# Performance work log

Hardware: AMD Instinct MI355X
Metric: run time of the kernel (lower is better)

Reference implementation:

```python
import jax, jax.numpy as jnp
import numpy as np

B, LK, H = 32, 4096, 512

def setup_inputs() -> dict:
    key = jax.random.key(0)
    ks = jax.random.split(key, 9)
    s = 1.0 / np.sqrt(H)
    return {
        "query": jax.random.normal(ks[0], (B, 1, H), jnp.float32),
        "keys": jax.random.normal(ks[1], (B, LK, H), jnp.float32),
        "Wa_w": jax.random.uniform(ks[2], (H, H), jnp.float32, -s, s),
        "Wa_b": jax.random.uniform(ks[3], (H,), jnp.float32, -s, s),
        "Ua_w": jax.random.uniform(ks[4], (H, H), jnp.float32, -s, s),
        "Ua_b": jax.random.uniform(ks[5], (H,), jnp.float32, -s, s),
        "Va_w": jax.random.uniform(ks[6], (1, H), jnp.float32, -s, s),
        "Va_b": jax.random.uniform(ks[7], (1,), jnp.float32, -s, s),
        "temperature": jnp.ones((1,), jnp.float32),
        "valid_src_len": jax.random.randint(ks[8], (B,), 1, LK + 1, jnp.int32),
    }

def reference(query, keys, Wa_w, Wa_b, Ua_w, Ua_b, Va_w, Va_b, temperature, valid_src_len):
    Lk = keys.shape[1]
    q = query @ Wa_w.T + Wa_b                      # [B,1,H]
    k = keys @ Ua_w.T + Ua_b                       # [B,Lk,H]
    # additive score: Va(tanh(Wa q + Ua k)) / T -> [B,Lk,1]
    scores = (jnp.tanh(q + k) @ Va_w.T + Va_b) / temperature
    scores = scores[..., 0][:, None, :]            # [B,1,Lk]
    mask = jnp.arange(Lk)[None, None, :] < valid_src_len[:, None, None]
    scores = jnp.where(mask, scores, jnp.asarray(-1e9, scores.dtype))
    weights = jax.nn.softmax(scores, axis=-1)      # [B,1,Lk]
    context = jnp.einsum('bql,blh->bqh', weights, keys)  # [B,1,H]
    return context, weights
```

## Files before the change

### kernel.cpp

```cpp
#include <hip/hip_runtime.h>

#define B_SZ 32
#define LK   4096
#define H    512
#define MT   64
#define AST  1040

typedef __bf16 bf16x8 __attribute__((ext_vector_type(8)));
typedef float  f32x4  __attribute__((ext_vector_type(4)));

__device__ inline unsigned short f2bf_rne(float f) {
    unsigned int u = __float_as_uint(f);
    u += 0x7FFFu + ((u >> 16) & 1u);
    return (unsigned short)(u >> 16);
}
__device__ inline unsigned pack_trunc(float lo, float hi) {
    return __builtin_amdgcn_perm(__float_as_uint(hi), __float_as_uint(lo), 0x07060302u);
}
__device__ inline float tanh_fast(float x) {
    float e = __expf(2.0f * x);
    return 1.0f - 2.0f * __builtin_amdgcn_rcpf(e + 1.0f);
}

__global__ void cvt_ua_kernel(const float* __restrict__ Ua_w, unsigned short* __restrict__ ua_t) {
    int n = blockIdx.x;
    int t = threadIdx.x;
    float2 f = *(const float2*)(Ua_w + n * H + t * 2);
    unsigned w = (unsigned)f2bf_rne(f.x) | ((unsigned)f2bf_rne(f.y) << 16);
    int k8 = t >> 2, off = t & 3;
    *(unsigned*)(ua_t + (size_t)k8 * (H * 8) + n * 8 + off * 2) = w;
}

__global__ void qproj_kernel(const float* __restrict__ query, const float* __restrict__ Wa_w,
                             const float* __restrict__ Wa_b, const float* __restrict__ Ua_b,
                             float* __restrict__ qadd) {
    __shared__ float qs[H];
    int b = blockIdx.x >> 3;
    int hseg = (blockIdx.x & 7) * 64;
    int t = threadIdx.x, wave = t >> 6, lane = t & 63;
    qs[t] = query[b * H + t];
    qs[t + 256] = query[b * H + t + 256];
    __syncthreads();
    for (int i = 0; i < 16; ++i) {
        int h = hseg + wave * 16 + i;
        const float* wr = Wa_w + (size_t)h * H + lane * 8;
        float4 a = *(const float4*)wr;
        float4 c = *(const float4*)(wr + 4);
        const float* q8 = qs + lane * 8;
        float s = a.x * q8[0] + a.y * q8[1] + a.z * q8[2] + a.w * q8[3]
                + c.x * q8[4] + c.y * q8[5] + c.z * q8[6] + c.w * q8[7];
        s += __shfl_xor(s, 1);  s += __shfl_xor(s, 2);  s += __shfl_xor(s, 4);
        s += __shfl_xor(s, 8);  s += __shfl_xor(s, 16); s += __shfl_xor(s, 32);
        if (lane == 0) qadd[b * H + h] = s + Wa_b[h] + Ua_b[h];
    }
}

__global__ __launch_bounds__(512, 2)
void main_kernel(const float* __restrict__ keys, const unsigned short* __restrict__ ua_t,
                 const float* __restrict__ qadd, const float* __restrict__ va_w,
                 const float* __restrict__ va_b, const float* __restrict__ temp,
                 const int* __restrict__ valid, float* __restrict__ p_out,
                 float* __restrict__ pc_part, float* __restrict__ psum_part) {
    __shared__ __align__(16) unsigned char alds[64 * AST];
    __shared__ __align__(16) unsigned char blds[2][32768];
    __shared__ float swave[8][32];
    __shared__ float pbuf[MT];

    const int blk  = blockIdx.x;
    const int b    = blk >> 6;
    const int m0   = (blk & 63) * MT;
    const int t    = threadIdx.x;
    const int wave = t >> 6;
    const int lane = t & 63;
    const int lrow = lane & 15;
    const int lquad = lane >> 4;
    const int wm   = wave >> 2;
    const int wn   = wave & 3;

    const float* keys_b = keys + ((size_t)b * LK + m0) * H;

    auto issueB = [&](int kc, int buf) {
        const unsigned short* slab = ua_t + (size_t)kc * (4 * 512 * 8);
        #pragma unroll
        for (int it = 0; it < 4; ++it) {
            int i = it * 512 + t;
            __builtin_amdgcn_global_load_lds(
                (const __attribute__((address_space(1))) void*)(slab + (size_t)i * 8),
                (__attribute__((address_space(3))) void*)(blds[buf] + i * 16),
                16, 0, 0);
        }
    };

    const int sh   = t & 1;
    const int sq   = (t >> 1) & 3;
    const int srow = t >> 3;
    const float* a_src = keys_b + (size_t)srow * H + sq * 8 + sh * 4;
    unsigned char* a_dst = alds + sq * AST + srow * 16 + sh * 8;

    float4 fa = *(const float4*)a_src;
    issueB(0, 0);
    {
        uint2 w;
        w.x = pack_trunc(fa.x, fa.y);
        w.y = pack_trunc(fa.z, fa.w);
        *(uint2*)a_dst = w;
    }

    float va[8], qa[8];
    #pragma unroll
    for (int nt = 0; nt < 8; ++nt) {
        int n = wn * 128 + nt * 16 + lrow;
        va[nt] = va_w[n];
        qa[nt] = qadd[b * H + n];
    }

    f32x4 acc[2][8];
    #pragma unroll
    for (int mt = 0; mt < 2; ++mt)
        #pragma unroll
        for (int nt = 0; nt < 8; ++nt)
            acc[mt][nt] = (f32x4){0.f, 0.f, 0.f, 0.f};

    __syncthreads();

    for (int kc = 0; kc < 16; ++kc) {
        float4 fnext;
        if (kc < 15) {
            fnext = *(const float4*)(a_src + (kc + 1) * 32);
            issueB(kc + 1, (kc + 1) & 1);
        }

        bf16x8 af[2];
        #pragma unroll
        for (int mt = 0; mt < 2; ++mt)
            af[mt] = *(const bf16x8*)(alds + (kc * 4 + lquad) * AST + (wm * 32 + mt * 16 + lrow) * 16);
        const unsigned char* bbase = blds[kc & 1];
        #pragma unroll
        for (int nt = 0; nt < 8; ++nt) {
            int n = wn * 128 + nt * 16 + lrow;
            bf16x8 bfrag = *(const bf16x8*)(bbase + (lquad * 512 + n) * 16);
            acc[0][nt] = __builtin_amdgcn_mfma_f32_16x16x32_bf16(af[0], bfrag, acc[0][nt], 0, 0, 0);
            acc[1][nt] = __builtin_amdgcn_mfma_f32_16x16x32_bf16(af[1], bfrag, acc[1][nt], 0, 0, 0);
        }

        if (kc < 15) {
            uint2 w;
            w.x = pack_trunc(fnext.x, fnext.y);
            w.y = pack_trunc(fnext.z, fnext.w);
            *(uint2*)(a_dst + (size_t)(kc + 1) * 4 * AST) = w;
        }
        __syncthreads();
    }

    #pragma unroll
    for (int mt = 0; mt < 2; ++mt) {
        #pragma unroll
        for (int r = 0; r < 4; ++r) {
            float s = 0.f;
            #pragma unroll
            for (int nt = 0; nt < 8; ++nt)
                s += tanh_fast(acc[mt][nt][r] + qa[nt]) * va[nt];
            s += __shfl_xor(s, 1); s += __shfl_xor(s, 2);
            s += __shfl_xor(s, 4); s += __shfl_xor(s, 8);
            if (lrow == 0) swave[wave][mt * 16 + lquad * 4 + r] = s;
        }
    }
    __syncthreads();

    if (t < MT) {
        int wmt = t >> 5, idx = t & 31;
        float score = (swave[wmt * 4 + 0][idx] + swave[wmt * 4 + 1][idx]
                     + swave[wmt * 4 + 2][idx] + swave[wmt * 4 + 3][idx] + va_b[0]) / temp[0];
        int l = m0 + t;
        float p = (l < valid[b]) ? __expf(score) : 0.f;
        p_out[(size_t)b * LK + l] = p;
        pbuf[t] = p;
        float s = p;
        s += __shfl_xor(s, 1);  s += __shfl_xor(s, 2);  s += __shfl_xor(s, 4);
        s += __shfl_xor(s, 8);  s += __shfl_xor(s, 16); s += __shfl_xor(s, 32);
        if (t == 0) psum_part[blk] = s;
    }
    __syncthreads();

    {
        float* red = (float*)blds;
        int oct = t & 63, rg = t >> 6;
        float s8[8];
        #pragma unroll
        for (int j = 0; j < 8; ++j) s8[j] = 0.f;
        #pragma unroll
        for (int rr = 0; rr < 8; ++rr) {
            int row = rg * 8 + rr;
            bf16x8 kv = *(const bf16x8*)(alds + oct * AST + row * 16);
            float pr = pbuf[row];
            #pragma unroll
            for (int j = 0; j < 8; ++j)
                s8[j] += pr * (float)kv[j];
        }
        #pragma unroll
        for (int j = 0; j < 8; ++j)
            red[rg * H + oct * 8 + j] = s8[j];
    }
    __syncthreads();
    {
        const float* red = (const float*)blds;
        float s = 0.f;
        #pragma unroll
        for (int rg = 0; rg < 8; ++rg)
            s += red[rg * H + t];
        pc_part[(size_t)blk * H + t] = s;
    }
}

__global__ void finalize_kernel(const float* __restrict__ p, const float* __restrict__ pc_part,
                                const float* __restrict__ psum_part, float* __restrict__ out) {
    int b = blockIdx.x / 18;
    int seg = blockIdx.x % 18;
    int t = threadIdx.x;
    __shared__ float tmp;
    if (t < 64) {
        float v = psum_part[b * 64 + t];
        v += __shfl_xor(v, 1);  v += __shfl_xor(v, 2);  v += __shfl_xor(v, 4);
        v += __shfl_xor(v, 8);  v += __shfl_xor(v, 16); v += __shfl_xor(v, 32);
        if (t == 0) tmp = v;
    }
    __syncthreads();
    float inv = 1.0f / tmp;
    if (seg < 16) {
        int l = seg * 256 + t;
        out[B_SZ * H + (size_t)b * LK + l] = p[(size_t)b * LK + l] * inv;
    } else {
        int h = (seg - 16) * 256 + t;
        float s = 0.f;
        #pragma unroll 8
        for (int i = 0; i < 64; ++i)
            s += pc_part[((size_t)b * 64 + i) * H + h];
        out[b * H + h] = s * inv;
    }
}

extern "C" void kernel_launch(void* const* d_in, const int* in_sizes, int n_in,
                              void* d_out, int out_size, void* d_ws, size_t ws_size,
                              hipStream_t stream) {
    const float* query = (const float*)d_in[0];
    const float* keys  = (const float*)d_in[1];
    const float* Wa_w  = (const float*)d_in[2];
    const float* Wa_b  = (const float*)d_in[3];
    const float* Ua_w  = (const float*)d_in[4];
    const float* Ua_b  = (const float*)d_in[5];
    const float* Va_w  = (const float*)d_in[6];
    const float* Va_b  = (const float*)d_in[7];
    const float* temp  = (const float*)d_in[8];
    const int*   valid = (const int*)d_in[9];
    float* out = (float*)d_out;

    char* ws = (char*)d_ws;
    unsigned short* ua_t = (unsigned short*)ws;
    float* qadd      = (float*)(ws + 524288);
    float* p         = (float*)(ws + 589824);
    float* psum_part = (float*)(ws + 1114112);
    float* pc_part   = (float*)(ws + 1122304);

    cvt_ua_kernel<<<H, 256, 0, stream>>>(Ua_w, ua_t);
    qproj_kernel<<<B_SZ * 8, 256, 0, stream>>>(query, Wa_w, Wa_b, Ua_b, qadd);
    main_kernel<<<B_SZ * (LK / MT), 512, 0, stream>>>(keys, ua_t, qadd, Va_w, Va_b,
                                                      temp, valid, p, pc_part, psum_part);
    finalize_kernel<<<B_SZ * 18, 256, 0, stream>>>(p, pc_part, psum_part, out);
}
```

Measured before the change: 492.4 us.

## Triple-buffer weight slabs and deepen key prefetch with manual waitcnt scheduling

Moves the weight-slab LDS staging from double to triple buffering. Keeps three key chunks in flight in registers using inline-asm global loads, and replaces the per-iteration __syncthreads with explicit vmcnt/lgkmcnt waits plus a raw s_barrier. The padded A layout is replaced by an XOR-swizzled 1KB-stride layout to avoid LDS bank conflicts without padding, and MFMA sections get raised wave priority. The aim is to hide global-load latency in the latency-bound GEMM loop. In exchange it uses hand-tuned wait counts that are fragile, and it takes the full 160KB of LDS.

Measured after the change: 459.1 us. 1.07x faster.

```diff
diff --git a/kernel.cpp b/kernel.cpp
--- a/kernel.cpp
+++ b/kernel.cpp
@@ -4,7 +4,6 @@
 #define LK   4096
 #define H    512
 #define MT   64
-#define AST  1040
 
 typedef __bf16 bf16x8 __attribute__((ext_vector_type(8)));
 typedef float  f32x4  __attribute__((ext_vector_type(4)));
@@ -61,10 +60,12 @@
                  const float* __restrict__ va_b, const float* __restrict__ temp,
                  const int* __restrict__ valid, float* __restrict__ p_out,
                  float* __restrict__ pc_part, float* __restrict__ psum_part) {
-    __shared__ __align__(16) unsigned char alds[64 * AST];
-    __shared__ __align__(16) unsigned char blds[2][32768];
-    __shared__ float swave[8][32];
-    __shared__ float pbuf[MT];
+    __shared__ __align__(16) unsigned char lds[163840];
+    unsigned char* alds = lds;
+    unsigned char* blds = lds + 65536;
+    float* red   = (float*)(lds + 65536);
+    float* swave = (float*)(lds + 65536 + 16384);
+    float* pbuf  = (float*)(lds + 65536 + 17408);
 
     const int blk  = blockIdx.x;
     const int b    = blk >> 6;
@@ -81,12 +82,13 @@
 
     auto issueB = [&](int kc, int buf) {
         const unsigned short* slab = ua_t + (size_t)kc * (4 * 512 * 8);
+        unsigned char* dst = blds + buf * 32768;
         #pragma unroll
         for (int it = 0; it < 4; ++it) {
             int i = it * 512 + t;
             __builtin_amdgcn_global_load_lds(
                 (const __attribute__((address_space(1))) void*)(slab + (size_t)i * 8),
-                (__attribute__((address_space(3))) void*)(blds[buf] + i * 16),
+                (__attribute__((address_space(3))) void*)(dst + i * 16),
                 16, 0, 0);
         }
     };
@@ -95,16 +97,14 @@
     const int sq   = (t >> 1) & 3;
     const int srow = t >> 3;
     const float* a_src = keys_b + (size_t)srow * H + sq * 8 + sh * 4;
-    unsigned char* a_dst = alds + sq * AST + srow * 16 + sh * 8;
-
-    float4 fa = *(const float4*)a_src;
-    issueB(0, 0);
-    {
+
+    auto packA = [&](int c, f32x4 f) {
         uint2 w;
-        w.x = pack_trunc(fa.x, fa.y);
-        w.y = pack_trunc(fa.z, fa.w);
-        *(uint2*)a_dst = w;
-    }
+        w.x = pack_trunc(f[0], f[1]);
+        w.y = pack_trunc(f[2], f[3]);
+        int k8 = c * 4 + sq;
+        *(uint2*)(alds + k8 * 1024 + ((srow * 16) ^ ((k8 & 7) << 4)) + sh * 8) = w;
+    };
 
     float va[8], qa[8];
     #pragma unroll
@@ -113,6 +113,18 @@
         va[nt] = va_w[n];
         qa[nt] = qadd[b * H + n];
     }
+    const int   valid_b = valid[b];
+    const float tv      = temp[0];
+    const float vab     = va_b[0];
+    asm volatile("s_waitcnt vmcnt(0) lgkmcnt(0)" ::: "memory");
+    __builtin_amdgcn_sched_barrier(0);
+
+    f32x4 fa[3];
+    asm volatile("global_load_dwordx4 %0, %1, off" : "=v"(fa[0]) : "v"(a_src));
+    asm volatile("global_load_dwordx4 %0, %1, off" : "=v"(fa[1]) : "v"(a_src + 32));
+    issueB(0, 0);
+    asm volatile("global_load_dwordx4 %0, %1, off" : "=v"(fa[2]) : "v"(a_src + 64));
+    issueB(1, 1);
 
     f32x4 acc[2][8];
     #pragma unroll
@@ -121,20 +133,31 @@
         for (int nt = 0; nt < 8; ++nt)
             acc[mt][nt] = (f32x4){0.f, 0.f, 0.f, 0.f};
 
-    __syncthreads();
-
-    for (int kc = 0; kc < 16; ++kc) {
-        float4 fnext;
-        if (kc < 15) {
-            fnext = *(const float4*)(a_src + (kc + 1) * 32);
-            issueB(kc + 1, (kc + 1) & 1);
-        }
+    asm volatile("s_waitcnt vmcnt(10)" ::: "memory");
+    __builtin_amdgcn_sched_barrier(0);
+    packA(0, fa[0]);
+    asm volatile("s_waitcnt vmcnt(5)" ::: "memory");
+    asm volatile("s_waitcnt lgkmcnt(0)" ::: "memory");
+    __builtin_amdgcn_sched_barrier(0);
+    __builtin_amdgcn_s_barrier();
+
+    #pragma unroll
+    for (int j = 0; j < 16; ++j) {
+        if (j < 15) packA(j + 1, fa[(j + 1) % 3]);
+        if (j <= 12)
+            asm volatile("global_load_dwordx4 %0, %1, off"
+                         : "=v"(fa[j % 3]) : "v"(a_src + (j + 3) * 32));
+        if (j <= 13) issueB(j + 2, (j + 2) % 3);
 
         bf16x8 af[2];
         #pragma unroll
-        for (int mt = 0; mt < 2; ++mt)
-            af[mt] = *(const bf16x8*)(alds + (kc * 4 + lquad) * AST + (wm * 32 + mt * 16 + lrow) * 16);
-        const unsigned char* bbase = blds[kc & 1];
+        for (int mt = 0; mt < 2; ++mt) {
+            int k8 = j * 4 + lquad;
+            int row16 = (wm * 32 + mt * 16 + lrow) * 16;
+            af[mt] = *(const bf16x8*)(alds + k8 * 1024 + (row16 ^ ((k8 & 7) << 4)));
+        }
+        const unsigned char* bbase = blds + (j % 3) * 32768;
+        __builtin_amdgcn_s_setprio(1);
         #pragma unroll
         for (int nt = 0; nt < 8; ++nt) {
             int n = wn * 128 + nt * 16 + lrow;
@@ -142,14 +165,15 @@
             acc[0][nt] = __builtin_amdgcn_mfma_f32_16x16x32_bf16(af[0], bfrag, acc[0][nt], 0, 0, 0);
             acc[1][nt] = __builtin_amdgcn_mfma_f32_16x16x32_bf16(af[1], bfrag, acc[1][nt], 0, 0, 0);
         }
-
-        if (kc < 15) {
-            uint2 w;
-            w.x = pack_trunc(fnext.x, fnext.y);
-            w.y = pack_trunc(fnext.z, fnext.w);
-            *(uint2*)(a_dst + (size_t)(kc + 1) * 4 * AST) = w;
-        }
-        __syncthreads();
+        __builtin_amdgcn_s_setprio(0);
+
+        __builtin_amdgcn_sched_barrier(0);
+        asm volatile("s_waitcnt lgkmcnt(0)" ::: "memory");
+        if (j <= 12)      { asm volatile("s_waitcnt vmcnt(5)" ::: "memory"); }
+        else if (j == 13) { asm volatile("s_waitcnt vmcnt(4)" ::: "memory"); }
+        else              { asm volatile("s_waitcnt vmcnt(0)" ::: "memory"); }
+        __builtin_amdgcn_sched_barrier(0);
+        __builtin_amdgcn_s_barrier();
     }
 
     #pragma unroll
@@ -162,17 +186,18 @@
                 s += tanh_fast(acc[mt][nt][r] + qa[nt]) * va[nt];
             s += __shfl_xor(s, 1); s += __shfl_xor(s, 2);
             s += __shfl_xor(s, 4); s += __shfl_xor(s, 8);
-            if (lrow == 0) swave[wave][mt * 16 + lquad * 4 + r] = s;
+            if (lrow == 0) swave[wave * 32 + mt * 16 + lquad * 4 + r] = s;
         }
     }
     __syncthreads();
 
     if (t < MT) {
         int wmt = t >> 5, idx = t & 31;
-        float score = (swave[wmt * 4 + 0][idx] + swave[wmt * 4 + 1][idx]
-                     + swave[wmt * 4 + 2][idx] + swave[wmt * 4 + 3][idx] + va_b[0]) / temp[0];
+        float score = (swave[(wmt * 4 + 0) * 32 + idx] + swave[(wmt * 4 + 1) * 32 + idx]
+                     + swave[(wmt * 4 + 2) * 32 + idx] + swave[(wmt * 4 + 3) * 32 + idx]
+                     + vab) / tv;
         int l = m0 + t;
-        float p = (l < valid[b]) ? __expf(score) : 0.f;
+        float p = (l < valid_b) ? __expf(score) : 0.f;
         p_out[(size_t)b * LK + l] = p;
         pbuf[t] = p;
         float s = p;
@@ -183,27 +208,25 @@
     __syncthreads();
 
     {
-        float* red = (float*)blds;
         int oct = t & 63, rg = t >> 6;
         float s8[8];
         #pragma unroll
-        for (int j = 0; j < 8; ++j) s8[j] = 0.f;
+        for (int jj = 0; jj < 8; ++jj) s8[jj] = 0.f;
         #pragma unroll
         for (int rr = 0; rr < 8; ++rr) {
             int row = rg * 8 + rr;
-            bf16x8 kv = *(const bf16x8*)(alds + oct * AST + row * 16);
+            bf16x8 kv = *(const bf16x8*)(alds + oct * 1024 + ((row * 16) ^ ((oct & 7) << 4)));
             float pr = pbuf[row];
             #pragma unroll
-            for (int j = 0; j < 8; ++j)
-                s8[j] += pr * (float)kv[j];
-        }
-        #pragma unroll
-        for (int j = 0; j < 8; ++j)
-            red[rg * H + oct * 8 + j] = s8[j];
+            for (int jj = 0; jj < 8; ++jj)
+                s8[jj] += pr * (float)kv[jj];
+        }
+        #pragma unroll
+        for (int jj = 0; jj < 8; ++jj)
+            red[rg * H + oct * 8 + jj] = s8[jj];
     }
     __syncthreads();
     {
-        const float* red = (const float*)blds;
         float s = 0.f;
         #pragma unroll
         for (int rg = 0; rg < 8; ++rg)
```

## Load Ua fragments straight into registers and use 4 waves with XOR-swizzled A tile

Applied to the files above, without the earlier changes.

The main kernel goes from 8 waves to 4, so each wave covers all 64 rows and a 128-column slice. Each wave now loads its B (Ua) fragments directly from global memory into registers with double buffering, replacing the shared-memory staging through global_load_lds. The A tile uses an XOR-swizzled layout instead of padding, and the loop is fully unrolled with raw barriers and setprio around the MFMA blocks. Register pressure rises (a 128-entry accumulator plus B buffers), and each wave reloads B from L2 instead of sharing it through LDS.

Result: faster. 419.0 us (-14.9%).

```diff
diff --git a/kernel.cpp b/kernel.cpp
--- a/kernel.cpp
+++ b/kernel.cpp
@@ -4,7 +4,6 @@
 #define LK   4096
 #define H    512
 #define MT   64
-#define AST  1040
 
 typedef __bf16 bf16x8 __attribute__((ext_vector_type(8)));
 typedef float  f32x4  __attribute__((ext_vector_type(4)));
@@ -20,6 +19,9 @@
 __device__ inline float tanh_fast(float x) {
     float e = __expf(2.0f * x);
     return 1.0f - 2.0f * __builtin_amdgcn_rcpf(e + 1.0f);
+}
+__device__ inline int aoff(int k8, int row) {
+    return k8 * 1024 + ((row * 16) ^ (((k8 & 7) << 4) | ((k8 & 3) << 8)));
 }
 
 __global__ void cvt_ua_kernel(const float* __restrict__ Ua_w, unsigned short* __restrict__ ua_t) {
@@ -55,15 +57,15 @@
     }
 }
 
-__global__ __launch_bounds__(512, 2)
+__global__ __launch_bounds__(256, 2)
 void main_kernel(const float* __restrict__ keys, const unsigned short* __restrict__ ua_t,
                  const float* __restrict__ qadd, const float* __restrict__ va_w,
                  const float* __restrict__ va_b, const float* __restrict__ temp,
                  const int* __restrict__ valid, float* __restrict__ p_out,
                  float* __restrict__ pc_part, float* __restrict__ psum_part) {
-    __shared__ __align__(16) unsigned char alds[64 * AST];
-    __shared__ __align__(16) unsigned char blds[2][32768];
-    __shared__ float swave[8][32];
+    __shared__ __align__(16) unsigned char alds[65536];
+    __shared__ float red[4][H];
+    __shared__ float swave[4][MT];
     __shared__ float pbuf[MT];
 
     const int blk  = blockIdx.x;
@@ -74,86 +76,96 @@
     const int lane = t & 63;
     const int lrow = lane & 15;
     const int lquad = lane >> 4;
-    const int wm   = wave >> 2;
-    const int wn   = wave & 3;
 
     const float* keys_b = keys + ((size_t)b * LK + m0) * H;
 
-    auto issueB = [&](int kc, int buf) {
-        const unsigned short* slab = ua_t + (size_t)kc * (4 * 512 * 8);
-        #pragma unroll
-        for (int it = 0; it < 4; ++it) {
-            int i = it * 512 + t;
-            __builtin_amdgcn_global_load_lds(
-                (const __attribute__((address_space(1))) void*)(slab + (size_t)i * 8),
-                (__attribute__((address_space(3))) void*)(blds[buf] + i * 16),
-                16, 0, 0);
-        }
-    };
-
-    const int sh   = t & 1;
-    const int sq   = (t >> 1) & 3;
-    const int srow = t >> 3;
-    const float* a_src = keys_b + (size_t)srow * H + sq * 8 + sh * 4;
-    unsigned char* a_dst = alds + sq * AST + srow * 16 + sh * 8;
-
-    float4 fa = *(const float4*)a_src;
-    issueB(0, 0);
+    const int sq = t & 3, srow = t >> 2;
+    const float* a_src = keys_b + (size_t)srow * H + sq * 8;
+
+    const unsigned short* b_base = ua_t + (size_t)lquad * (H * 8) + (wave * 128 + lrow) * 8;
+
+    f32x4 fa[2][2];
+    fa[0][0] = *(const f32x4*)(a_src);
+    fa[0][1] = *(const f32x4*)(a_src + 4);
+    fa[1][0] = *(const f32x4*)(a_src + 32);
+    fa[1][1] = *(const f32x4*)(a_src + 36);
+    bf16x8 bb[2][8];
+    #pragma unroll
+    for (int nt = 0; nt < 8; ++nt)
+        bb[0][nt] = *(const bf16x8*)(b_base + nt * 128);
+
     {
-        uint2 w;
-        w.x = pack_trunc(fa.x, fa.y);
-        w.y = pack_trunc(fa.z, fa.w);
-        *(uint2*)a_dst = w;
+        uint4 w;
+        w.x = pack_trunc(fa[0][0][0], fa[0][0][1]);
+        w.y = pack_trunc(fa[0][0][2], fa[0][0][3]);
+        w.z = pack_trunc(fa[0][1][0], fa[0][1][1]);
+        w.w = pack_trunc(fa[0][1][2], fa[0][1][3]);
+        *(uint4*)(alds + aoff(sq, srow)) = w;
+    }
+
+    f32x4 acc[4][8];
+    #pragma unroll
+    for (int mt = 0; mt < 4; ++mt)
+        #pragma unroll
+        for (int nt = 0; nt < 8; ++nt)
+            acc[mt][nt] = (f32x4){0.f, 0.f, 0.f, 0.f};
+
+    asm volatile("s_waitcnt lgkmcnt(0)" ::: "memory");
+    __builtin_amdgcn_s_barrier();
+    __builtin_amdgcn_sched_barrier(0);
+
+    #pragma unroll
+    for (int j = 0; j < 16; ++j) {
+        if (j < 15) {
+            f32x4 lo = fa[(j + 1) & 1][0], hi = fa[(j + 1) & 1][1];
+            uint4 w;
+            w.x = pack_trunc(lo[0], lo[1]);
+            w.y = pack_trunc(lo[2], lo[3]);
+            w.z = pack_trunc(hi[0], hi[1]);
+            w.w = pack_trunc(hi[2], hi[3]);
+            *(uint4*)(alds + aoff((j + 1) * 4 + sq, srow)) = w;
+        }
+        if (j < 14) {
+            fa[j & 1][0] = *(const f32x4*)(a_src + (j + 2) * 32);
+            fa[j & 1][1] = *(const f32x4*)(a_src + (j + 2) * 32 + 4);
+        }
+        if (j < 15) {
+            #pragma unroll
+            for (int nt = 0; nt < 8; ++nt)
+                bb[(j + 1) & 1][nt] =
+                    *(const bf16x8*)(b_base + (size_t)(j + 1) * 16384 + nt * 128);
+        }
+
+        __builtin_amdgcn_s_setprio(1);
+        #pragma unroll
+        for (int mt = 0; mt < 4; ++mt) {
+            int k8 = j * 4 + lquad;
+            bf16x8 af = *(const bf16x8*)(alds + aoff(k8, mt * 16 + lrow));
+            #pragma unroll
+            for (int nt = 0; nt < 8; ++nt)
+                acc[mt][nt] = __builtin_amdgcn_mfma_f32_16x16x32_bf16(
+                    af, bb[j & 1][nt], acc[mt][nt], 0, 0, 0);
+        }
+        __builtin_amdgcn_s_setprio(0);
+
+        if (j < 15) {
+            __builtin_amdgcn_sched_barrier(0);
+            asm volatile("s_waitcnt lgkmcnt(0)" ::: "memory");
+            __builtin_amdgcn_s_barrier();
+            __builtin_amdgcn_sched_barrier(0);
+        }
     }
 
     float va[8], qa[8];
     #pragma unroll
     for (int nt = 0; nt < 8; ++nt) {
-        int n = wn * 128 + nt * 16 + lrow;
+        int n = wave * 128 + nt * 16 + lrow;
         va[nt] = va_w[n];
         qa[nt] = qadd[b * H + n];
     }
 
-    f32x4 acc[2][8];
-    #pragma unroll
-    for (int mt = 0; mt < 2; ++mt)
-        #pragma unroll
-        for (int nt = 0; nt < 8; ++nt)
-            acc[mt][nt] = (f32x4){0.f, 0.f, 0.f, 0.f};
-
-    __syncthreads();
-
-    for (int kc = 0; kc < 16; ++kc) {
-        float4 fnext;
-        if (kc < 15) {
-            fnext = *(const float4*)(a_src + (kc + 1) * 32);
-            issueB(kc + 1, (kc + 1) & 1);
-        }
-
-        bf16x8 af[2];
-        #pragma unroll
-        for (int mt = 0; mt < 2; ++mt)
-            af[mt] = *(const bf16x8*)(alds + (kc * 4 + lquad) * AST + (wm * 32 + mt * 16 + lrow) * 16);
-        const unsigned char* bbase = blds[kc & 1];
-        #pragma unroll
-        for (int nt = 0; nt < 8; ++nt) {
-            int n = wn * 128 + nt * 16 + lrow;
-            bf16x8 bfrag = *(const bf16x8*)(bbase + (lquad * 512 + n) * 16);
-            acc[0][nt] = __builtin_amdgcn_mfma_f32_16x16x32_bf16(af[0], bfrag, acc[0][nt], 0, 0, 0);
-            acc[1][nt] = __builtin_amdgcn_mfma_f32_16x16x32_bf16(af[1], bfrag, acc[1][nt], 0, 0, 0);
-        }
-
-        if (kc < 15) {
-            uint2 w;
-            w.x = pack_trunc(fnext.x, fnext.y);
-            w.y = pack_trunc(fnext.z, fnext.w);
-            *(uint2*)(a_dst + (size_t)(kc + 1) * 4 * AST) = w;
-        }
-        __syncthreads();
-    }
-
-    #pragma unroll
-    for (int mt = 0; mt < 2; ++mt) {
+    #pragma unroll
+    for (int mt = 0; mt < 4; ++mt) {
         #pragma unroll
         for (int r = 0; r < 4; ++r) {
             float s = 0.f;
@@ -168,9 +180,8 @@
     __syncthreads();
 
     if (t < MT) {
-        int wmt = t >> 5, idx = t & 31;
-        float score = (swave[wmt * 4 + 0][idx] + swave[wmt * 4 + 1][idx]
-                     + swave[wmt * 4 + 2][idx] + swave[wmt * 4 + 3][idx] + va_b[0]) / temp[0];
+        float score = (swave[0][t] + swave[1][t] + swave[2][t] + swave[3][t]
+                     + va_b[0]) / temp[0];
         int l = m0 + t;
         float p = (l < valid[b]) ? __expf(score) : 0.f;
         p_out[(size_t)b * LK + l] = p;
@@ -183,32 +194,30 @@
     __syncthreads();
 
     {
-        float* red = (float*)blds;
         int oct = t & 63, rg = t >> 6;
         float s8[8];
         #pragma unroll
-        for (int j = 0; j < 8; ++j) s8[j] = 0.f;
-        #pragma unroll
-        for (int rr = 0; rr < 8; ++rr) {
-            int row = rg * 8 + rr;
-            bf16x8 kv = *(const bf16x8*)(alds + oct * AST + row * 16);
+        for (int jj = 0; jj < 8; ++jj) s8[jj] = 0.f;
+        #pragma unroll
+        for (int rr = 0; rr < 16; ++rr) {
+            int row = rg * 16 + rr;
+            bf16x8 kv = *(const bf16x8*)(alds + aoff(oct, row));
             float pr = pbuf[row];
             #pragma unroll
-            for (int j = 0; j < 8; ++j)
-                s8[j] += pr * (float)kv[j];
-        }
-        #pragma unroll
-        for (int j = 0; j < 8; ++j)
-            red[rg * H + oct * 8 + j] = s8[j];
+            for (int jj = 0; jj < 8; ++jj)
+                s8[jj] += pr * (float)kv[jj];
+        }
+        #pragma unroll
+        for (int jj = 0; jj < 8; ++jj)
+            red[rg][oct * 8 + jj] = s8[jj];
     }
     __syncthreads();
     {
-        const float* red = (const float*)blds;
-        float s = 0.f;
-        #pragma unroll
-        for (int rg = 0; rg < 8; ++rg)
-            s += red[rg * H + t];
-        pc_part[(size_t)blk * H + t] = s;
+        #pragma unroll
+        for (int rep = 0; rep < 2; ++rep) {
+            int h = t + rep * 256;
+            pc_part[(size_t)blk * H + h] = red[0][h] + red[1][h] + red[2][h] + red[3][h];
+        }
     }
 }
 
@@ -263,7 +272,7 @@
 
     cvt_ua_kernel<<<H, 256, 0, stream>>>(Ua_w, ua_t);
     qproj_kernel<<<B_SZ * 8, 256, 0, stream>>>(query, Wa_w, Wa_b, Ua_b, qadd);
-    main_kernel<<<B_SZ * (LK / MT), 512, 0, stream>>>(keys, ua_t, qadd, Va_w, Va_b,
+    main_kernel<<<B_SZ * (LK / MT), 256, 0, stream>>>(keys, ua_t, qadd, Va_w, Va_b,
                                                       temp, valid, p, pc_part, psum_part);
     finalize_kernel<<<B_SZ * 18, 256, 0, stream>>>(p, pc_part, psum_part, out);
 }
```
